# Performance work log

Measured on AMD Instinct MI355X. Metric: run time of the kernel, lower is better.

## Reference

```python
import jax, jax.numpy as jnp
import numpy as np

N_NODES = 100000
N_EDGES = 400000
N_GRAPHS = 4096
BN_EPS = 1e-5


def _glorot(key, shape):
    fan_in, fan_out = shape
    lim = np.sqrt(6.0 / (fan_in + fan_out))
    return jax.random.uniform(key, shape, jnp.float32, -lim, lim)


def setup_inputs() -> dict:
    key = jax.random.key(0)
    ks = jax.random.split(key, 16)
    x = jax.random.normal(ks[0], (N_NODES, 373), jnp.float32)
    edge_index = jax.random.randint(ks[1], (2, N_EDGES), 0, N_NODES, jnp.int64)
    batch = jnp.sort(jax.random.randint(ks[2], (N_NODES,), 0, N_GRAPHS, jnp.int64))
    params = {
        # GIN layer 1 MLP: 373->256->256
        'W1a': _glorot(ks[3], (373, 256)), 'b1a': jnp.zeros((256,), jnp.float32),
        'W1b': _glorot(ks[4], (256, 256)), 'b1b': jnp.zeros((256,), jnp.float32),
        'g1': jnp.ones((256,), jnp.float32), 'be1': jnp.zeros((256,), jnp.float32),
        # GIN layer 2 MLP: 256->128->128
        'W2a': _glorot(ks[5], (256, 128)), 'b2a': jnp.zeros((128,), jnp.float32),
        'W2b': _glorot(ks[6], (128, 128)), 'b2b': jnp.zeros((128,), jnp.float32),
        'g2': jnp.ones((128,), jnp.float32), 'be2': jnp.zeros((128,), jnp.float32),
        # GIN layer 3 MLP: 128->64->64
        'W3a': _glorot(ks[7], (128, 64)), 'b3a': jnp.zeros((64,), jnp.float32),
        'W3b': _glorot(ks[8], (64, 64)), 'b3b': jnp.zeros((64,), jnp.float32),
        'g3': jnp.ones((64,), jnp.float32), 'be3': jnp.zeros((64,), jnp.float32),
        # head
        'Wf1': _glorot(ks[9], (64, 16)), 'bf1': jnp.zeros((16,), jnp.float32),
        'Wf2': _glorot(ks[10], (16, 1)), 'bf2': jnp.zeros((1,), jnp.float32),
    }
    return {'x': x, 'edge_index': edge_index, 'batch': batch, **params}


def _gin_conv(x, src, dst, Wa, ba, Wb, bb):
    # sum-aggregate neighbor messages (eps = 0 default in GINConv)
    agg = jax.ops.segment_sum(x[src], dst, num_segments=N_NODES)
    h = x + agg
    h = jax.nn.relu(h @ Wa + ba) @ Wb + bb
    return h


def _batchnorm(x, gamma, beta):
    mu = jnp.mean(x, axis=0)
    var = jnp.var(x, axis=0)
    return (x - mu) * jax.lax.rsqrt(var + BN_EPS) * gamma + beta


def reference(x, edge_index, batch,
              W1a, b1a, W1b, b1b, g1, be1,
              W2a, b2a, W2b, b2b, g2, be2,
              W3a, b3a, W3b, b3b, g3, be3,
              Wf1, bf1, Wf2, bf2):
    src, dst = edge_index[0], edge_index[1]
    h = jax.nn.relu(_gin_conv(x, src, dst, W1a, b1a, W1b, b1b))
    h = _batchnorm(h, g1, be1)
    h = jax.nn.relu(_gin_conv(h, src, dst, W2a, b2a, W2b, b2b))
    h = _batchnorm(h, g2, be2)
    h = jax.nn.relu(_gin_conv(h, src, dst, W3a, b3a, W3b, b3b))
    h = _batchnorm(h, g3, be3)
    # global_add_pool: [N, 64] -> [G, 64]
    pooled = jax.ops.segment_sum(h, batch, num_segments=N_GRAPHS)
    out = jax.nn.relu(pooled @ Wf1 + bf1)
    # dropout omitted (eval mode)
    out = jax.nn.relu(out @ Wf2 + bf2)
    return out.reshape(-1)
```

## Files before the change

### kernel.cpp

```cpp
#include <hip/hip_runtime.h>

#define N_NODES 100000
#define N_EDGES 400000
#define N_GRAPHS 4096
#define BN_EPS 1e-5f
#define DEG_CAP 96

typedef unsigned short ushort_t;
typedef short short8 __attribute__((ext_vector_type(8)));
typedef unsigned short ushort4v __attribute__((ext_vector_type(4)));
typedef float floatx4 __attribute__((ext_vector_type(4)));

__device__ __forceinline__ ushort_t f2b(float f) {
    union { float f; unsigned u; } v; v.f = f;
    unsigned r = v.u + 0x7fffu + ((v.u >> 16) & 1u);
    return (ushort_t)(r >> 16);
}
__device__ __forceinline__ float b2f(ushort_t b) {
    union { unsigned u; float f; } v; v.u = ((unsigned)b) << 16;
    return v.f;
}

__global__ void k_pad_x(const float* __restrict__ x, ushort_t* __restrict__ xb) {
    int n = blockIdx.x;
    int t = threadIdx.x;
    const float* xr = x + (long)n * 373;
    ushort_t* o = xb + (long)n * 384;
    if (t < 93) {
        float v0 = xr[t * 4 + 0], v1 = xr[t * 4 + 1], v2 = xr[t * 4 + 2], v3 = xr[t * 4 + 3];
        ushort4v s = {f2b(v0), f2b(v1), f2b(v2), f2b(v3)};
        *(ushort4v*)(o + t * 4) = s;
    } else if (t == 93) {
        o[372] = f2b(xr[372]);
        o[373] = 0; o[374] = 0; o[375] = 0;
    } else if (t == 94 || t == 95) {
        ushort4v z = {0, 0, 0, 0};
        *(ushort4v*)(o + 376 + (t - 94) * 4) = z;
    }
}

__global__ void k_zero_int(int* __restrict__ p, int n) {
    int i = blockIdx.x * blockDim.x + threadIdx.x;
    if (i < n) p[i] = 0;
}

__global__ void k_fill(const int* __restrict__ src, const int* __restrict__ dst,
                       int* __restrict__ cursor, int* __restrict__ elist) {
    int e = blockIdx.x * blockDim.x + threadIdx.x;
    if (e < N_EDGES) {
        int d = dst[e];
        int slot = atomicAdd(&cursor[d], 1);
        if (slot < DEG_CAP) elist[(long)d * DEG_CAP + slot] = src[e];
    }
}

__global__ void k_prep_bt(const float* __restrict__ W, const float* __restrict__ sc,
                          ushort_t* __restrict__ BT, int K, int Kp, int Nn) {
    int k = blockIdx.x * 128 + threadIdx.x;
    int n = blockIdx.y;
    if (k >= Kp) return;
    float v = 0.f;
    if (k < K) { v = W[(long)k * Nn + n]; if (sc) v *= sc[k]; }
    BT[(long)n * Kp + k] = f2b(v);
}

__global__ void k_bias_eff(const float* __restrict__ W, const float* __restrict__ sh,
                           float* __restrict__ out, int K, int Nn) {
    int n = blockIdx.x * blockDim.x + threadIdx.x;
    if (n >= Nn) return;
    float s = 0.f;
    for (int k = 0; k < K; k++) s += sh[k] * W[(long)k * Nn + n];
    out[n] = s;
}

template<int KP, int TN, bool STATS>
__global__ __launch_bounds__(256) void k_gemm(const ushort_t* __restrict__ A,
                                              const ushort_t* __restrict__ BT,
                                              const float* __restrict__ bias,
                                              ushort_t* __restrict__ C,
                                              float* __restrict__ partials,
                                              int M, int Nn, int relu) {
    __shared__ __align__(16) ushort_t As[128 * 32];
    __shared__ __align__(16) ushort_t Bs[TN * 32];
    __shared__ float swred[STATS ? 4 * 2 * TN : 1];
    const int tid = threadIdx.x;
    const int wave = tid >> 6, lane = tid & 63;
    const int ln = lane & 15, kg = lane >> 4;
    const long rowBase = (long)blockIdx.y * 128;
    const int colBase = blockIdx.x * TN;

    constexpr int RT = (TN == 128) ? 4 : 2;
    const int rowOff = (TN == 128) ? ((wave >> 1) * 64) : (wave * 32);
    const int colOff = (TN == 128) ? ((wave & 1) * 64) : 0;

    const ushort_t* aSrc[2];
#pragma unroll
    for (int i = 0; i < 2; i++) {
        long r = rowBase + i * 64 + (tid >> 2);
        if (r >= M) r = M - 1;
        aSrc[i] = A + r * KP + (tid & 3) * 8;
    }
    const ushort_t* bSrc[TN / 64];
#pragma unroll
    for (int i = 0; i < TN / 64; i++) {
        long cc = colBase + i * 64 + (tid >> 2);
        bSrc[i] = BT + cc * KP + (tid & 3) * 8;
    }
    ushort_t* aDst = As + wave * 512;
    ushort_t* bDst = Bs + wave * 512;

    floatx4 acc[RT][4];
#pragma unroll
    for (int i = 0; i < RT; i++)
#pragma unroll
        for (int j = 0; j < 4; j++) acc[i][j] = (floatx4){0.f, 0.f, 0.f, 0.f};

    for (int k0 = 0; k0 < KP; k0 += 32) {
        __syncthreads();
#pragma unroll
        for (int i = 0; i < 2; i++)
            __builtin_amdgcn_global_load_lds(
                (const __attribute__((address_space(1))) void*)(aSrc[i] + k0),
                (__attribute__((address_space(3))) void*)(aDst + i * 2048), 16, 0, 0);
#pragma unroll
        for (int i = 0; i < TN / 64; i++)
            __builtin_amdgcn_global_load_lds(
                (const __attribute__((address_space(1))) void*)(bSrc[i] + k0),
                (__attribute__((address_space(3))) void*)(bDst + i * 2048), 16, 0, 0);
        __syncthreads();

        short8 afr[RT], bfr[4];
#pragma unroll
        for (int rt = 0; rt < RT; rt++)
            afr[rt] = *(const short8*)&As[(rowOff + rt * 16 + ln) * 32 + kg * 8];
#pragma unroll
        for (int tn = 0; tn < 4; tn++)
            bfr[tn] = *(const short8*)&Bs[(colOff + tn * 16 + ln) * 32 + kg * 8];
#pragma unroll
        for (int rt = 0; rt < RT; rt++)
#pragma unroll
            for (int tn = 0; tn < 4; tn++)
                acc[rt][tn] = __builtin_amdgcn_mfma_f32_16x16x32_bf16(afr[rt], bfr[tn], acc[rt][tn], 0, 0, 0);
    }

    if constexpr (STATS) {
        for (int i = tid; i < 4 * 2 * TN; i += 256) swred[i] = 0.f;
        __syncthreads();
    }

    float sums[4] = {0.f, 0.f, 0.f, 0.f};
    float sqs[4]  = {0.f, 0.f, 0.f, 0.f};
#pragma unroll
    for (int rt = 0; rt < RT; rt++) {
#pragma unroll
        for (int tn = 0; tn < 4; tn++) {
            int gc = colBase + colOff + tn * 16 + ln;
            float bv = bias ? bias[gc] : 0.f;
#pragma unroll
            for (int r = 0; r < 4; r++) {
                long gr = rowBase + rowOff + rt * 16 + kg * 4 + r;
                if (gr < M) {
                    float v = acc[rt][tn][r] + bv;
                    if (relu) v = fmaxf(v, 0.f);
                    ushort_t sb = f2b(v);
                    C[gr * Nn + gc] = sb;
                    if (STATS) {
                        float vb = b2f(sb);
                        sums[tn] += vb;
                        sqs[tn] += vb * vb;
                    }
                }
            }
        }
    }
    if constexpr (STATS) {
#pragma unroll
        for (int tn = 0; tn < 4; tn++) {
            float s = sums[tn], q = sqs[tn];
            s += __shfl_xor(s, 16); q += __shfl_xor(q, 16);
            s += __shfl_xor(s, 32); q += __shfl_xor(q, 32);
            if (kg == 0) {
                int c = colOff + tn * 16 + ln;
                swred[wave * 2 * TN + c] = s;
                swred[wave * 2 * TN + TN + c] = q;
            }
        }
        __syncthreads();
        const int by = blockIdx.y;
        const int gyd = gridDim.y;
        for (int c = tid; c < TN; c += 256) {
            float ssum = 0.f, ssq = 0.f;
#pragma unroll
            for (int w = 0; w < 4; w++) {
                ssum += swred[w * 2 * TN + c];
                ssq  += swred[w * 2 * TN + TN + c];
            }
            long gc = colBase + c;
            partials[gc * gyd + by] = ssum;
            partials[((long)Nn + gc) * gyd + by] = ssq;
        }
    }
}

__global__ void k_stats_reduce(const float* __restrict__ partials,
                               float* __restrict__ stats, int gy) {
    int col = blockIdx.x;
    int lane = threadIdx.x;
    const float* p = partials + (long)col * gy;
    float s = 0.f;
    for (int i = lane; i < gy; i += 64) s += p[i];
#pragma unroll
    for (int off = 32; off >= 1; off >>= 1) s += __shfl_xor(s, off);
    if (lane == 0) stats[col] = s;
}

template<int D>
__global__ void k_aggregate(const ushort_t* __restrict__ y, const int* __restrict__ cursor,
                            const int* __restrict__ elist, const float* __restrict__ badd,
                            ushort_t* __restrict__ out) {
    const int CG = D / 4;
    const int NPB = 64 / CG;
    int t = threadIdx.x;
    int n = blockIdx.x * NPB + t / CG;
    int c = (t % CG) * 4;
    if (n >= N_NODES) return;
    int cnt = cursor[n];
    if (cnt > DEG_CAP) cnt = DEG_CAP;
    ushort4v sv = *(const ushort4v*)(y + (long)n * D + c);
    float t0 = b2f(sv.x), t1 = b2f(sv.y), t2 = b2f(sv.z), t3 = b2f(sv.w);
    const int* el = elist + (long)n * DEG_CAP;
    if (cnt > 0) {
        long s0 = el[0];
        ushort4v nv = *(const ushort4v*)(y + s0 * D + c);
        for (int i = 1; i <= cnt; i++) {
            ushort4v cur = nv;
            if (i < cnt) {
                long s = el[i];
                nv = *(const ushort4v*)(y + s * D + c);
            }
            t0 += b2f(cur.x); t1 += b2f(cur.y); t2 += b2f(cur.z); t3 += b2f(cur.w);
        }
    }
    t0 = fmaxf(t0 + badd[c + 0], 0.f);
    t1 = fmaxf(t1 + badd[c + 1], 0.f);
    t2 = fmaxf(t2 + badd[c + 2], 0.f);
    t3 = fmaxf(t3 + badd[c + 3], 0.f);
    ushort4v o = {f2b(t0), f2b(t1), f2b(t2), f2b(t3)};
    *(ushort4v*)(out + (long)n * D + c) = o;
}

__global__ void k_bn_finalize(const float* __restrict__ stats, const float* __restrict__ gamma,
                              const float* __restrict__ beta, float* __restrict__ scsh, int K) {
    int c = threadIdx.x;
    if (c < K) {
        float invN = 1.0f / (float)N_NODES;
        float mu = stats[c] * invN;
        float var = fmaxf(stats[K + c] * invN - mu * mu, 0.f);
        float sc = rsqrtf(var + BN_EPS) * gamma[c];
        scsh[c] = sc;
        scsh[K + c] = beta[c] - mu * sc;
    }
}

__global__ void k_pool(const ushort_t* __restrict__ h, const int* __restrict__ batch,
                       const float* __restrict__ scsh, float* __restrict__ pooled) {
    int g = blockIdx.x;
    int c = threadIdx.x;
    int lo = 0, hi = N_NODES;
    while (lo < hi) { int mid = (lo + hi) >> 1; if (batch[mid] < g) lo = mid + 1; else hi = mid; }
    int start = lo;
    hi = N_NODES;
    while (lo < hi) { int mid = (lo + hi) >> 1; if (batch[mid] < g + 1) lo = mid + 1; else hi = mid; }
    int end = lo;
    float s = 0.f;
    for (int r = start; r < end; r++) s += b2f(h[(long)r * 64 + c]);
    pooled[g * 64 + c] = s * scsh[c] + scsh[64 + c] * (float)(end - start);
}

__global__ void k_head(const float* __restrict__ pooled, const float* __restrict__ Wf1,
                       const float* __restrict__ bf1, const float* __restrict__ Wf2,
                       const float* __restrict__ bf2, float* __restrict__ out) {
    int g = blockIdx.x * blockDim.x + threadIdx.x;
    if (g >= N_GRAPHS) return;
    const float* p = pooled + g * 64;
    float o = 0.f;
#pragma unroll
    for (int k = 0; k < 16; k++) {
        float s = bf1[k];
        for (int c = 0; c < 64; c++) s += p[c] * Wf1[c * 16 + k];
        s = fmaxf(s, 0.f);
        o += s * Wf2[k];
    }
    o += bf2[0];
    o = fmaxf(o, 0.f);
    out[g] = o;
}

extern "C" void kernel_launch(void* const* d_in, const int* in_sizes, int n_in,
                              void* d_out, int out_size, void* d_ws, size_t ws_size,
                              hipStream_t stream) {
    const float* x    = (const float*)d_in[0];
    const int*  ei    = (const int*)d_in[1];
    const int*  batch = (const int*)d_in[2];
    const float* W1a = (const float*)d_in[3];
    const float* b1a = (const float*)d_in[4];
    const float* W1b = (const float*)d_in[5];
    const float* b1b = (const float*)d_in[6];
    const float* g1  = (const float*)d_in[7];
    const float* be1 = (const float*)d_in[8];
    const float* W2a = (const float*)d_in[9];
    const float* b2a = (const float*)d_in[10];
    const float* W2b = (const float*)d_in[11];
    const float* b2b = (const float*)d_in[12];
    const float* g2  = (const float*)d_in[13];
    const float* be2 = (const float*)d_in[14];
    const float* W3a = (const float*)d_in[15];
    const float* b3a = (const float*)d_in[16];
    const float* W3b = (const float*)d_in[17];
    const float* b3b = (const float*)d_in[18];
    const float* g3  = (const float*)d_in[19];
    const float* be3 = (const float*)d_in[20];
    const float* Wf1 = (const float*)d_in[21];
    const float* bf1 = (const float*)d_in[22];
    const float* Wf2 = (const float*)d_in[23];
    const float* bf2 = (const float*)d_in[24];

    const int N = N_NODES, E = N_EDGES;
    const int* src = ei;
    const int* dst = ei + E;
    const int gy = (N + 127) / 128;

    char* wp = (char*)d_ws;
    auto carve = [&](size_t bytes) {
        char* p = wp;
        wp += (bytes + 255) & ~(size_t)255;
        return (void*)p;
    };
    ushort_t* xb     = (ushort_t*)carve((size_t)N * 384 * 2);
    ushort_t* bufA   = (ushort_t*)carve((size_t)N * 256 * 2);
    ushort_t* bufB   = (ushort_t*)carve((size_t)N * 256 * 2);
    int*      elist  = (int*)carve((size_t)N * DEG_CAP * 4);
    int*      cursor = (int*)carve((size_t)N * 4);
    ushort_t* BT     = (ushort_t*)carve((size_t)256 * 384 * 2);
    float*    stats  = (float*)carve(1536 * 4);
    float*    scsh   = (float*)carve(512 * 4);
    float*    biasE  = (float*)carve(256 * 4);
    float*    pooled = (float*)carve((size_t)N_GRAPHS * 64 * 4);
    float*    partials = (float*)carve((size_t)2 * 256 * gy * 4);

    dim3 blk(256);

    k_pad_x<<<N, 128, 0, stream>>>(x, xb);
    k_zero_int<<<(N + 255) / 256, blk, 0, stream>>>(cursor, N);
    k_fill<<<(E + 255) / 256, blk, 0, stream>>>(src, dst, cursor, elist);

    k_prep_bt<<<dim3(3, 256), 128, 0, stream>>>(W1a, nullptr, BT, 373, 384, 256);
    k_gemm<384, 128, false><<<dim3(2, gy), blk, 0, stream>>>(xb, BT, nullptr, bufA, nullptr, N, 256, 0);
    k_aggregate<256><<<N, 64, 0, stream>>>(bufA, cursor, elist, b1a, bufB);
    k_prep_bt<<<dim3(2, 256), 128, 0, stream>>>(W1b, nullptr, BT, 256, 256, 256);
    k_gemm<256, 128, true><<<dim3(2, gy), blk, 0, stream>>>(bufB, BT, b1b, bufA, partials, N, 256, 1);
    k_stats_reduce<<<512, 64, 0, stream>>>(partials, stats, gy);
    k_bn_finalize<<<1, blk, 0, stream>>>(stats, g1, be1, scsh, 256);

    k_prep_bt<<<dim3(2, 128), 128, 0, stream>>>(W2a, scsh, BT, 256, 256, 128);
    k_bias_eff<<<1, 128, 0, stream>>>(W2a, scsh + 256, biasE, 256, 128);
    k_gemm<256, 128, false><<<dim3(1, gy), blk, 0, stream>>>(bufA, BT, biasE, bufB, nullptr, N, 128, 0);
    k_aggregate<128><<<(N + 1) / 2, 64, 0, stream>>>(bufB, cursor, elist, b2a, bufA);
    k_prep_bt<<<dim3(1, 128), 128, 0, stream>>>(W2b, nullptr, BT, 128, 128, 128);
    k_gemm<128, 128, true><<<dim3(1, gy), blk, 0, stream>>>(bufA, BT, b2b, bufB, partials, N, 128, 1);
    k_stats_reduce<<<256, 64, 0, stream>>>(partials, stats + 512, gy);
    k_bn_finalize<<<1, blk, 0, stream>>>(stats + 512, g2, be2, scsh, 128);

    k_prep_bt<<<dim3(1, 64), 128, 0, stream>>>(W3a, scsh, BT, 128, 128, 64);
    k_bias_eff<<<1, 64, 0, stream>>>(W3a, scsh + 128, biasE, 128, 64);
    k_gemm<128, 64, false><<<dim3(1, gy), blk, 0, stream>>>(bufB, BT, biasE, bufA, nullptr, N, 64, 0);
    k_aggregate<64><<<(N + 3) / 4, 64, 0, stream>>>(bufA, cursor, elist, b3a, bufB);
    k_prep_bt<<<dim3(1, 64), 128, 0, stream>>>(W3b, nullptr, BT, 64, 64, 64);
    k_gemm<64, 64, true><<<dim3(1, gy), blk, 0, stream>>>(bufB, BT, b3b, bufA, partials, N, 64, 1);
    k_stats_reduce<<<128, 64, 0, stream>>>(partials, stats + 1024, gy);
    k_bn_finalize<<<1, blk, 0, stream>>>(stats + 1024, g3, be3, scsh, 64);

    k_pool<<<N_GRAPHS, 64, 0, stream>>>(bufA, batch, scsh, pooled);
    k_head<<<(N_GRAPHS + 255) / 256, blk, 0, stream>>>(pooled, Wf1, bf1, Wf2, bf2, (float*)d_out);
}
```

Baseline: 756.7 us.

## Fuse aggregation into second GEMM and merge small prep kernels to cut launches

Layers 2 and 3 now run neighbor aggregation straight into a swizzled shared-memory A tile and feed it to MFMA in the same kernel. This drops the aggregate kernel's output write and the GEMM's reload of it. Weight transposes, cursor zeroing, stats reduction plus BN finalize, bias folding, and pool plus head are each merged into neighboring kernels, which cuts the launch count roughly in half. The aggregation loop is also unrolled by two to keep more gathers in flight. In exchange the fused kernel uses a large LDS tile (128xKP) and does uneven gather work per block, which may hurt occupancy and balance.

Result: faster. 672.0 us (-11.2%).

```diff
diff --git a/kernel.cpp b/kernel.cpp
--- a/kernel.cpp
+++ b/kernel.cpp
@@ -9,6 +9,7 @@
 typedef unsigned short ushort_t;
 typedef short short8 __attribute__((ext_vector_type(8)));
 typedef unsigned short ushort4v __attribute__((ext_vector_type(4)));
+typedef unsigned short ushort8v __attribute__((ext_vector_type(8)));
 typedef float floatx4 __attribute__((ext_vector_type(4)));
 
 __device__ __forceinline__ ushort_t f2b(float f) {
@@ -21,9 +22,19 @@
     return v.f;
 }
 
-__global__ void k_pad_x(const float* __restrict__ x, ushort_t* __restrict__ xb) {
+__global__ void k_pad_x(const float* __restrict__ x, ushort_t* __restrict__ xb,
+                        int* __restrict__ cursor,
+                        const float* __restrict__ W1a, ushort_t* __restrict__ BT1) {
+    int t = threadIdx.x;
+    if (blockIdx.x >= N_NODES) {
+        int b = blockIdx.x - N_NODES;
+        int n = b / 3, kc = b % 3;
+        int k = kc * 128 + t;
+        float v = (k < 373) ? W1a[(long)k * 256 + n] : 0.f;
+        BT1[(long)n * 384 + k] = f2b(v);
+        return;
+    }
     int n = blockIdx.x;
-    int t = threadIdx.x;
     const float* xr = x + (long)n * 373;
     ushort_t* o = xb + (long)n * 384;
     if (t < 93) {
@@ -36,12 +47,9 @@
     } else if (t == 94 || t == 95) {
         ushort4v z = {0, 0, 0, 0};
         *(ushort4v*)(o + 376 + (t - 94) * 4) = z;
-    }
-}
-
-__global__ void k_zero_int(int* __restrict__ p, int n) {
-    int i = blockIdx.x * blockDim.x + threadIdx.x;
-    if (i < n) p[i] = 0;
+    } else if (t == 96) {
+        cursor[n] = 0;
+    }
 }
 
 __global__ void k_fill(const int* __restrict__ src, const int* __restrict__ dst,
@@ -54,23 +62,25 @@
     }
 }
 
-__global__ void k_prep_bt(const float* __restrict__ W, const float* __restrict__ sc,
-                          ushort_t* __restrict__ BT, int K, int Kp, int Nn) {
+__global__ void k_prep_scaled(const float* __restrict__ W, const float* __restrict__ scsh,
+                              ushort_t* __restrict__ BT, float* __restrict__ biasE,
+                              int K, int Kp, int Nn) {
+    int n = blockIdx.y;
     int k = blockIdx.x * 128 + threadIdx.x;
-    int n = blockIdx.y;
-    if (k >= Kp) return;
-    float v = 0.f;
-    if (k < K) { v = W[(long)k * Nn + n]; if (sc) v *= sc[k]; }
-    BT[(long)n * Kp + k] = f2b(v);
-}
-
-__global__ void k_bias_eff(const float* __restrict__ W, const float* __restrict__ sh,
-                           float* __restrict__ out, int K, int Nn) {
-    int n = blockIdx.x * blockDim.x + threadIdx.x;
-    if (n >= Nn) return;
-    float s = 0.f;
-    for (int k = 0; k < K; k++) s += sh[k] * W[(long)k * Nn + n];
-    out[n] = s;
+    if (k < Kp) {
+        float v = (k < K) ? W[(long)k * Nn + n] * scsh[k] : 0.f;
+        BT[(long)n * Kp + k] = f2b(v);
+    }
+    if (blockIdx.x == 0) {
+        __shared__ float red[2];
+        float s = 0.f;
+        for (int kk = threadIdx.x; kk < K; kk += 128) s += scsh[K + kk] * W[(long)kk * Nn + n];
+#pragma unroll
+        for (int off = 32; off >= 1; off >>= 1) s += __shfl_xor(s, off);
+        if ((threadIdx.x & 63) == 0) red[threadIdx.x >> 6] = s;
+        __syncthreads();
+        if (threadIdx.x == 0) biasE[n] = red[0] + red[1];
+    }
 }
 
 template<int KP, int TN, bool STATS>
@@ -202,25 +212,178 @@
     }
 }
 
-__global__ void k_stats_reduce(const float* __restrict__ partials,
-                               float* __restrict__ stats, int gy) {
-    int col = blockIdx.x;
-    int lane = threadIdx.x;
-    const float* p = partials + (long)col * gy;
-    float s = 0.f;
-    for (int i = lane; i < gy; i += 64) s += p[i];
-#pragma unroll
-    for (int off = 32; off >= 1; off >>= 1) s += __shfl_xor(s, off);
-    if (lane == 0) stats[col] = s;
+template<int KP, int TN>
+__global__ __launch_bounds__(256) void k_gemm_agg(const ushort_t* __restrict__ y,
+                                                  const int* __restrict__ cursor,
+                                                  const int* __restrict__ elist,
+                                                  const float* __restrict__ badd,
+                                                  const ushort_t* __restrict__ BT,
+                                                  const float* __restrict__ bias,
+                                                  ushort_t* __restrict__ C,
+                                                  float* __restrict__ partials,
+                                                  int M, int Nn) {
+    __shared__ __align__(16) ushort_t Af[128 * KP];
+    __shared__ __align__(16) ushort_t Bs[TN * 32];
+    __shared__ float swred[4 * 2 * TN];
+    const int tid = threadIdx.x;
+    const int wave = tid >> 6, lane = tid & 63;
+    const int ln = lane & 15, kg = lane >> 4;
+    const long rowBase = (long)blockIdx.y * 128;
+    constexpr int CPR = KP / 8;
+    constexpr int TPR = CPR;
+    constexpr int RPS = 256 / TPR;
+
+    {
+        const int lr = tid / TPR;
+        const int ck = tid % TPR;
+        const int c0 = ck * 8;
+        float bd[8];
+#pragma unroll
+        for (int j = 0; j < 8; j++) bd[j] = badd[c0 + j];
+        for (int s = 0; s < 128; s += RPS) {
+            int r = s + lr;
+            long gr = rowBase + r; if (gr >= M) gr = M - 1;
+            int cnt = cursor[gr]; if (cnt > DEG_CAP) cnt = DEG_CAP;
+            const int* el = elist + gr * DEG_CAP;
+            ushort8v sv = *(const ushort8v*)(y + gr * KP + c0);
+            float av[8];
+#pragma unroll
+            for (int j = 0; j < 8; j++) av[j] = b2f(sv[j]);
+            if (cnt > 0) {
+                ushort8v va = *(const ushort8v*)(y + (long)el[0] * KP + c0);
+                ushort8v vb = va;
+                if (cnt > 1) vb = *(const ushort8v*)(y + (long)el[1] * KP + c0);
+                for (int i = 0; i < cnt; i += 2) {
+                    ushort8v u0 = va, u1 = vb;
+                    if (i + 2 < cnt) va = *(const ushort8v*)(y + (long)el[i + 2] * KP + c0);
+                    if (i + 3 < cnt) vb = *(const ushort8v*)(y + (long)el[i + 3] * KP + c0);
+#pragma unroll
+                    for (int j = 0; j < 8; j++) av[j] += b2f(u0[j]);
+                    if (i + 1 < cnt) {
+#pragma unroll
+                        for (int j = 0; j < 8; j++) av[j] += b2f(u1[j]);
+                    }
+                }
+            }
+            ushort8v ov;
+#pragma unroll
+            for (int j = 0; j < 8; j++) ov[j] = f2b(fmaxf(av[j] + bd[j], 0.f));
+            int cks = ck ^ (r & (CPR - 1));
+            *(ushort8v*)&Af[r * KP + cks * 8] = ov;
+        }
+    }
+
+    constexpr int RT = (TN == 128) ? 4 : 2;
+    const int rowOff = (TN == 128) ? ((wave >> 1) * 64) : (wave * 32);
+    const int colOff = (TN == 128) ? ((wave & 1) * 64) : 0;
+    const ushort_t* bSrc[TN / 64];
+#pragma unroll
+    for (int i = 0; i < TN / 64; i++) {
+        long cc = i * 64 + (tid >> 2);
+        bSrc[i] = BT + cc * KP + (tid & 3) * 8;
+    }
+    ushort_t* bDst = Bs + wave * 512;
+
+    floatx4 acc[RT][4];
+#pragma unroll
+    for (int i = 0; i < RT; i++)
+#pragma unroll
+        for (int j = 0; j < 4; j++) acc[i][j] = (floatx4){0.f, 0.f, 0.f, 0.f};
+
+    for (int k0 = 0; k0 < KP; k0 += 32) {
+        __syncthreads();
+#pragma unroll
+        for (int i = 0; i < TN / 64; i++)
+            __builtin_amdgcn_global_load_lds(
+                (const __attribute__((address_space(1))) void*)(bSrc[i] + k0),
+                (__attribute__((address_space(3))) void*)(bDst + i * 2048), 16, 0, 0);
+        __syncthreads();
+
+        short8 afr[RT], bfr[4];
+#pragma unroll
+        for (int rt = 0; rt < RT; rt++) {
+            int row = rowOff + rt * 16 + ln;
+            int cks = ((k0 >> 3) + kg) ^ (row & (CPR - 1));
+            afr[rt] = *(const short8*)&Af[row * KP + cks * 8];
+        }
+#pragma unroll
+        for (int tn = 0; tn < 4; tn++)
+            bfr[tn] = *(const short8*)&Bs[(colOff + tn * 16 + ln) * 32 + kg * 8];
+#pragma unroll
+        for (int rt = 0; rt < RT; rt++)
+#pragma unroll
+            for (int tn = 0; tn < 4; tn++)
+                acc[rt][tn] = __builtin_amdgcn_mfma_f32_16x16x32_bf16(afr[rt], bfr[tn], acc[rt][tn], 0, 0, 0);
+    }
+
+    for (int i = tid; i < 4 * 2 * TN; i += 256) swred[i] = 0.f;
+    __syncthreads();
+
+    float sums[4] = {0.f, 0.f, 0.f, 0.f};
+    float sqs[4]  = {0.f, 0.f, 0.f, 0.f};
+#pragma unroll
+    for (int rt = 0; rt < RT; rt++) {
+#pragma unroll
+        for (int tn = 0; tn < 4; tn++) {
+            int gc = colOff + tn * 16 + ln;
+            float bv = bias[gc];
+#pragma unroll
+            for (int r = 0; r < 4; r++) {
+                long gr = rowBase + rowOff + rt * 16 + kg * 4 + r;
+                if (gr < M) {
+                    float v = fmaxf(acc[rt][tn][r] + bv, 0.f);
+                    ushort_t sb = f2b(v);
+                    C[gr * Nn + gc] = sb;
+                    float vb = b2f(sb);
+                    sums[tn] += vb;
+                    sqs[tn] += vb * vb;
+                }
+            }
+        }
+    }
+#pragma unroll
+    for (int tn = 0; tn < 4; tn++) {
+        float s = sums[tn], q = sqs[tn];
+        s += __shfl_xor(s, 16); q += __shfl_xor(q, 16);
+        s += __shfl_xor(s, 32); q += __shfl_xor(q, 32);
+        if (kg == 0) {
+            int c = colOff + tn * 16 + ln;
+            swred[wave * 2 * TN + c] = s;
+            swred[wave * 2 * TN + TN + c] = q;
+        }
+    }
+    __syncthreads();
+    const int by = blockIdx.y;
+    const int gyd = gridDim.y;
+    for (int c = tid; c < TN; c += 256) {
+        float ssum = 0.f, ssq = 0.f;
+#pragma unroll
+        for (int w = 0; w < 4; w++) {
+            ssum += swred[w * 2 * TN + c];
+            ssq  += swred[w * 2 * TN + TN + c];
+        }
+        partials[(long)c * gyd + by] = ssum;
+        partials[((long)Nn + c) * gyd + by] = ssq;
+    }
 }
 
 template<int D>
 __global__ void k_aggregate(const ushort_t* __restrict__ y, const int* __restrict__ cursor,
                             const int* __restrict__ elist, const float* __restrict__ badd,
-                            ushort_t* __restrict__ out) {
+                            ushort_t* __restrict__ out, int nblk,
+                            const float* __restrict__ Wn, ushort_t* __restrict__ BTn,
+                            int KWn, int NWn) {
+    int t = threadIdx.x;
+    if ((int)blockIdx.x >= nblk) {
+        int b = blockIdx.x - nblk;
+        int nk = KWn >> 6;
+        int n = b / nk, kc = b - n * nk;
+        int k = kc * 64 + t;
+        BTn[(long)n * KWn + k] = f2b(Wn[(long)k * NWn + n]);
+        return;
+    }
     const int CG = D / 4;
     const int NPB = 64 / CG;
-    int t = threadIdx.x;
     int n = blockIdx.x * NPB + t / CG;
     int c = (t % CG) * 4;
     if (n >= N_NODES) return;
@@ -230,15 +393,17 @@
     float t0 = b2f(sv.x), t1 = b2f(sv.y), t2 = b2f(sv.z), t3 = b2f(sv.w);
     const int* el = elist + (long)n * DEG_CAP;
     if (cnt > 0) {
-        long s0 = el[0];
-        ushort4v nv = *(const ushort4v*)(y + s0 * D + c);
-        for (int i = 1; i <= cnt; i++) {
-            ushort4v cur = nv;
-            if (i < cnt) {
-                long s = el[i];
-                nv = *(const ushort4v*)(y + s * D + c);
+        ushort4v va = *(const ushort4v*)(y + (long)el[0] * D + c);
+        ushort4v vb = va;
+        if (cnt > 1) vb = *(const ushort4v*)(y + (long)el[1] * D + c);
+        for (int i = 0; i < cnt; i += 2) {
+            ushort4v u0 = va, u1 = vb;
+            if (i + 2 < cnt) va = *(const ushort4v*)(y + (long)el[i + 2] * D + c);
+            if (i + 3 < cnt) vb = *(const ushort4v*)(y + (long)el[i + 3] * D + c);
+            t0 += b2f(u0.x); t1 += b2f(u0.y); t2 += b2f(u0.z); t3 += b2f(u0.w);
+            if (i + 1 < cnt) {
+                t0 += b2f(u1.x); t1 += b2f(u1.y); t2 += b2f(u1.z); t3 += b2f(u1.w);
             }
-            t0 += b2f(cur.x); t1 += b2f(cur.y); t2 += b2f(cur.z); t3 += b2f(cur.w);
         }
     }
     t0 = fmaxf(t0 + badd[c + 0], 0.f);
@@ -249,21 +414,44 @@
     *(ushort4v*)(out + (long)n * D + c) = o;
 }
 
-__global__ void k_bn_finalize(const float* __restrict__ stats, const float* __restrict__ gamma,
-                              const float* __restrict__ beta, float* __restrict__ scsh, int K) {
-    int c = threadIdx.x;
-    if (c < K) {
+__global__ void k_bn(const float* __restrict__ partials, int gy,
+                     const float* __restrict__ gamma, const float* __restrict__ beta,
+                     float* __restrict__ scsh, int K,
+                     const float* __restrict__ Wn, ushort_t* __restrict__ BTn,
+                     int KWn, int NWn) {
+    int b = blockIdx.x;
+    int t = threadIdx.x;
+    if (b >= K) {
+        int p = b - K;
+        int nk = KWn >> 6;
+        int n = p / nk, kc = p - n * nk;
+        int k = kc * 64 + t;
+        BTn[(long)n * KWn + k] = f2b(Wn[(long)k * NWn + n]);
+        return;
+    }
+    const float* ps = partials + (long)b * gy;
+    const float* pq = partials + (long)(K + b) * gy;
+    float s = 0.f, q = 0.f;
+    for (int i = t; i < gy; i += 64) { s += ps[i]; q += pq[i]; }
+#pragma unroll
+    for (int off = 32; off >= 1; off >>= 1) { s += __shfl_xor(s, off); q += __shfl_xor(q, off); }
+    if (t == 0) {
         float invN = 1.0f / (float)N_NODES;
-        float mu = stats[c] * invN;
-        float var = fmaxf(stats[K + c] * invN - mu * mu, 0.f);
-        float sc = rsqrtf(var + BN_EPS) * gamma[c];
-        scsh[c] = sc;
-        scsh[K + c] = beta[c] - mu * sc;
-    }
-}
-
-__global__ void k_pool(const ushort_t* __restrict__ h, const int* __restrict__ batch,
-                       const float* __restrict__ scsh, float* __restrict__ pooled) {
+        float mu = s * invN;
+        float var = fmaxf(q * invN - mu * mu, 0.f);
+        float sc = rsqrtf(var + BN_EPS) * gamma[b];
+        scsh[b] = sc;
+        scsh[K + b] = beta[b] - mu * sc;
+    }
+}
+
+__global__ void k_poolhead(const ushort_t* __restrict__ h, const int* __restrict__ batch,
+                           const float* __restrict__ scsh,
+                           const float* __restrict__ Wf1, const float* __restrict__ bf1,
+                           const float* __restrict__ Wf2, const float* __restrict__ bf2,
+                           float* __restrict__ out) {
+    __shared__ float pl[64];
+    __shared__ float hid[16];
     int g = blockIdx.x;
     int c = threadIdx.x;
     int lo = 0, hi = N_NODES;
@@ -274,26 +462,20 @@
     int end = lo;
     float s = 0.f;
     for (int r = start; r < end; r++) s += b2f(h[(long)r * 64 + c]);
-    pooled[g * 64 + c] = s * scsh[c] + scsh[64 + c] * (float)(end - start);
-}
-
-__global__ void k_head(const float* __restrict__ pooled, const float* __restrict__ Wf1,
-                       const float* __restrict__ bf1, const float* __restrict__ Wf2,
-                       const float* __restrict__ bf2, float* __restrict__ out) {
-    int g = blockIdx.x * blockDim.x + threadIdx.x;
-    if (g >= N_GRAPHS) return;
-    const float* p = pooled + g * 64;
-    float o = 0.f;
-#pragma unroll
-    for (int k = 0; k < 16; k++) {
-        float s = bf1[k];
-        for (int c = 0; c < 64; c++) s += p[c] * Wf1[c * 16 + k];
-        s = fmaxf(s, 0.f);
-        o += s * Wf2[k];
-    }
-    o += bf2[0];
-    o = fmaxf(o, 0.f);
-    out[g] = o;
+    pl[c] = s * scsh[c] + scsh[64 + c] * (float)(end - start);
+    __syncthreads();
+    if (c < 16) {
+        float sh = bf1[c];
+        for (int j = 0; j < 64; j++) sh += pl[j] * Wf1[j * 16 + c];
+        hid[c] = fmaxf(sh, 0.f);
+    }
+    __syncthreads();
+    if (c == 0) {
+        float o = bf2[0];
+#pragma unroll
+        for (int k = 0; k < 16; k++) o += hid[k] * Wf2[k];
+        out[g] = fmaxf(o, 0.f);
+    }
 }
 
 extern "C" void kernel_launch(void* const* d_in, const int* in_sizes, int n_in,
@@ -341,45 +523,31 @@
     ushort_t* bufB   = (ushort_t*)carve((size_t)N * 256 * 2);
     int*      elist  = (int*)carve((size_t)N * DEG_CAP * 4);
     int*      cursor = (int*)carve((size_t)N * 4);
-    ushort_t* BT     = (ushort_t*)carve((size_t)256 * 384 * 2);
-    float*    stats  = (float*)carve(1536 * 4);
+    ushort_t* BT1    = (ushort_t*)carve((size_t)256 * 384 * 2);
+    ushort_t* BT2    = (ushort_t*)carve((size_t)256 * 384 * 2);
     float*    scsh   = (float*)carve(512 * 4);
     float*    biasE  = (float*)carve(256 * 4);
-    float*    pooled = (float*)carve((size_t)N_GRAPHS * 64 * 4);
     float*    partials = (float*)carve((size_t)2 * 256 * gy * 4);
 
     dim3 blk(256);
 
-    k_pad_x<<<N, 128, 0, stream>>>(x, xb);
-    k_zero_int<<<(N + 255) / 256, blk, 0, stream>>>(cursor, N);
+    k_pad_x<<<N + 768, 128, 0, stream>>>(x, xb, cursor, W1a, BT1);
     k_fill<<<(E + 255) / 256, blk, 0, stream>>>(src, dst, cursor, elist);
 
-    k_prep_bt<<<dim3(3, 256), 128, 0, stream>>>(W1a, nullptr, BT, 373, 384, 256);
-    k_gemm<384, 128, false><<<dim3(2, gy), blk, 0, stream>>>(xb, BT, nullptr, bufA, nullptr, N, 256, 0);
-    k_aggregate<256><<<N, 64, 0, stream>>>(bufA, cursor, elist, b1a, bufB);
-    k_prep_bt<<<dim3(2, 256), 128, 0, stream>>>(W1b, nullptr, BT, 256, 256, 256);
-    k_gemm<256, 128, true><<<dim3(2, gy), blk, 0, stream>>>(bufB, BT, b1b, bufA, partials, N, 256, 1);
-    k_stats_reduce<<<512, 64, 0, stream>>>(partials, stats, gy);
-    k_bn_finalize<<<1, blk, 0, stream>>>(stats, g1, be1, scsh, 256);
-
-    k_prep_bt<<<dim3(2, 128), 128, 0, stream>>>(W2a, scsh, BT, 256, 256, 128);
-    k_bias_eff<<<1, 128, 0, stream>>>(W2a, scsh + 256, biasE, 256, 128);
-    k_gemm<256, 128, false><<<dim3(1, gy), blk, 0, stream>>>(bufA, BT, biasE, bufB, nullptr, N, 128, 0);
-    k_aggregate<128><<<(N + 1) / 2, 64, 0, stream>>>(bufB, cursor, elist, b2a, bufA);
-    k_prep_bt<<<dim3(1, 128), 128, 0, stream>>>(W2b, nullptr, BT, 128, 128, 128);
-    k_gemm<128, 128, true><<<dim3(1, gy), blk, 0, stream>>>(bufA, BT, b2b, bufB, partials, N, 128, 1);
-    k_stats_reduce<<<256, 64, 0, stream>>>(partials, stats + 512, gy);
-    k_bn_finalize<<<1, blk, 0, stream>>>(stats + 512, g2, be2, scsh, 128);
-
-    k_prep_bt<<<dim3(1, 64), 128, 0, stream>>>(W3a, scsh, BT, 128, 128, 64);
-    k_bias_eff<<<1, 64, 0, stream>>>(W3a, scsh + 128, biasE, 128, 64);
-    k_gemm<128, 64, false><<<dim3(1, gy), blk, 0, stream>>>(bufB, BT, biasE, bufA, nullptr, N, 64, 0);
-    k_aggregate<64><<<(N + 3) / 4, 64, 0, stream>>>(bufA, cursor, elist, b3a, bufB);
-    k_prep_bt<<<dim3(1, 64), 128, 0, stream>>>(W3b, nullptr, BT, 64, 64, 64);
-    k_gemm<64, 64, true><<<dim3(1, gy), blk, 0, stream>>>(bufB, BT, b3b, bufA, partials, N, 64, 1);
-    k_stats_reduce<<<128, 64, 0, stream>>>(partials, stats + 1024, gy);
-    k_bn_finalize<<<1, blk, 0, stream>>>(stats + 1024, g3, be3, scsh, 64);
-
-    k_pool<<<N_GRAPHS, 64, 0, stream>>>(bufA, batch, scsh, pooled);
-    k_head<<<(N_GRAPHS + 255) / 256, blk, 0, stream>>>(pooled, Wf1, bf1, Wf2, bf2, (float*)d_out);
-}
+    k_gemm<384, 128, false><<<dim3(2, gy), blk, 0, stream>>>(xb, BT1, nullptr, bufA, nullptr, N, 256, 0);
+    k_aggregate<256><<<N + 1024, 64, 0, stream>>>(bufA, cursor, elist, b1a, bufB, N, W1b, BT2, 256, 256);
+    k_gemm<256, 128, true><<<dim3(2, gy), blk, 0, stream>>>(bufB, BT2, b1b, bufA, partials, N, 256, 1);
+    k_bn<<<256 + 256, 64, 0, stream>>>(partials, gy, g1, be1, scsh, 256, W2b, BT2, 128, 128);
+
+    k_prep_scaled<<<dim3(2, 128), 128, 0, stream>>>(W2a, scsh, BT1, biasE, 256, 256, 128);
+    k_gemm<256, 128, false><<<dim3(1, gy), blk, 0, stream>>>(bufA, BT1, biasE, bufB, nullptr, N, 128, 0);
+    k_gemm_agg<128, 128><<<dim3(1, gy), blk, 0, stream>>>(bufB, cursor, elist, b2a, BT2, b2b, bufA, partials, N, 128);
+    k_bn<<<128 + 64, 64, 0, stream>>>(partials, gy, g2, be2, scsh, 128, W3b, BT2, 64, 64);
+
+    k_prep_scaled<<<dim3(1, 64), 128, 0, stream>>>(W3a, scsh, BT1, biasE, 128, 128, 64);
+    k_gemm<128, 64, false><<<dim3(1, gy), blk, 0, stream>>>(bufA, BT1, biasE, bufB, nullptr, N, 64, 0);
+    k_gemm_agg<64, 64><<<dim3(1, gy), blk, 0, stream>>>(bufB, cursor, elist, b3a, BT2, b3b, bufA, partials, N, 64);
+    k_bn<<<64, 64, 0, stream>>>(partials, gy, g3, be3, scsh, 64, nullptr, nullptr, 64, 64);
+
+    k_poolhead<<<N_GRAPHS, 64, 0, stream>>>(bufA, batch, scsh, Wf1, bf1, Wf2, bf2, (float*)d_out);
+}
```
